# Kernel optimization log

Hardware: AMD Instinct MI355X
Metric: run time of the kernel (lower is better)

## Reference

```python
import jax, jax.numpy as jnp
import numpy as np

_EPS = 1e-4  # pytorch3d se3_exp_map clamps the SQUARED rotation angle at this eps


def _hat(w):
    # w: [..., 3] -> skew-symmetric [..., 3, 3]
    wx, wy, wz = w[..., 0], w[..., 1], w[..., 2]
    z = jnp.zeros_like(wx)
    return jnp.stack([
        jnp.stack([z, -wz, wy], axis=-1),
        jnp.stack([wz, z, -wx], axis=-1),
        jnp.stack([-wy, wx, z], axis=-1),
    ], axis=-2)


def _se3_exp(dofs):
    # dofs: [..., 6] = (log_translation, log_rotation), pytorch3d convention.
    # Returns R [..., 3, 3] and t [..., 3] such that p' = R @ p + t,
    # matching pytorch3d's row-convention matrix M ([:3,:3]=R^T, [3,:3]=t)
    # applied as p' = p @ M[:3,:3] + M[3,:3].
    t_log = dofs[..., :3]
    w = dofs[..., 3:]
    nrms = jnp.sum(w * w, axis=-1)
    theta = jnp.sqrt(jnp.clip(nrms, _EPS))  # [...]
    H = _hat(w)
    H2 = H @ H
    st, ct = jnp.sin(theta), jnp.cos(theta)
    f1 = (st / theta)[..., None, None]
    f2 = ((1.0 - ct) / (theta * theta))[..., None, None]
    f3 = ((theta - st) / (theta * theta * theta))[..., None, None]
    I = jnp.eye(3, dtype=dofs.dtype)
    R = I + f1 * H + f2 * H2            # Rodrigues
    V = I + f2 * H + f3 * H2            # left-Jacobian of SO(3)
    t = jnp.einsum('...ij,...j->...i', V, t_log)
    return R, t


def setup_inputs() -> dict:
    key = jax.random.key(0)
    k1, k2 = jax.random.split(key)
    B, T, N = 64, 28, 4096
    X_v = jax.random.normal(k1, (B, T, N, 3), dtype=jnp.float32)
    dofs = jax.random.normal(k2, (B, T, 6), dtype=jnp.float32)
    return {"X_v": X_v, "dofs": dofs}


def reference(X_v, dofs):
    # Fused, fully-batched version of the per-tooth python loop:
    # one SE3 exp over all (B,T) transforms + one batched point transform.
    R, t = _se3_exp(dofs)                                  # [B,T,3,3], [B,T,3]
    out = jnp.einsum('btij,btnj->btni', R, X_v) + t[:, :, None, :]
    return out
```

## Files before the change

### kernel.cpp

```cpp
#include <hip/hip_runtime.h>


typedef float f4 __attribute__((ext_vector_type(4)));

__device__ __forceinline__ float rfl(float x) {
    return __uint_as_float(__builtin_amdgcn_readfirstlane(__float_as_uint(x)));
}

__global__ __launch_bounds__(256) void se3_apply_kernel(
    const float* __restrict__ X,
    const float* __restrict__ dofs,
    float* __restrict__ out,
    int n3,
    int tilesPerBT)
{
    const int bt   = blockIdx.x / tilesPerBT;
    const int tile = blockIdx.x - bt * tilesPerBT;
    const int t    = threadIdx.x;

    const int fInBT = tile * 3072 + t * 12;
    const long long baseF = (long long)bt * (long long)n3 + (long long)fInBT;
    const f4* __restrict__ Xp = (const f4*)(X + baseF);
    f4* __restrict__ Op       = (f4*)(out + baseF);

    const bool full = (fInBT + 12) <= n3;
    f4 v0, v1, v2;
    if (full) { v0 = Xp[0]; v1 = Xp[1]; v2 = Xp[2]; }

    const float* d = dofs + bt * 6;
    const float tx = d[0], ty = d[1], tz = d[2];
    const float wx = d[3], wy = d[4], wz = d[5];

    const float nrm2  = wx * wx + wy * wy + wz * wz;
    const float th2   = fmaxf(nrm2, 1e-4f);
    const float theta = sqrtf(th2);
    const float st = sinf(theta);
    const float ct = cosf(theta);
    const float f1 = st / theta;
    const float f2 = (1.0f - ct) / th2;
    const float f3 = (theta - st) / (th2 * theta);

    const float xx = wx * wx, yy = wy * wy, zz = wz * wz;
    const float xy = wx * wy, xz = wx * wz, yz = wy * wz;

    const float R00 = rfl(1.0f - f2 * (yy + zz));
    const float R01 = rfl(f2 * xy - f1 * wz);
    const float R02 = rfl(f2 * xz + f1 * wy);
    const float R10 = rfl(f2 * xy + f1 * wz);
    const float R11 = rfl(1.0f - f2 * (xx + zz));
    const float R12 = rfl(f2 * yz - f1 * wx);
    const float R20 = rfl(f2 * xz - f1 * wy);
    const float R21 = rfl(f2 * yz + f1 * wx);
    const float R22 = rfl(1.0f - f2 * (xx + yy));

    const float V00 = 1.0f - f3 * (yy + zz);
    const float V01 = f3 * xy - f2 * wz;
    const float V02 = f3 * xz + f2 * wy;
    const float V10 = f3 * xy + f2 * wz;
    const float V11 = 1.0f - f3 * (xx + zz);
    const float V12 = f3 * yz - f2 * wx;
    const float V20 = f3 * xz - f2 * wy;
    const float V21 = f3 * yz + f2 * wx;
    const float V22 = 1.0f - f3 * (xx + yy);

    const float Tx = rfl(V00 * tx + V01 * ty + V02 * tz);
    const float Ty = rfl(V10 * tx + V11 * ty + V12 * tz);
    const float Tz = rfl(V20 * tx + V21 * ty + V22 * tz);

    if (full) {
        const float x0 = v0.x, y0 = v0.y, z0 = v0.z;
        const float x1 = v0.w, y1 = v1.x, z1 = v1.y;
        const float x2 = v1.z, y2 = v1.w, z2 = v2.x;
        const float x3 = v2.y, y3 = v2.z, z3 = v2.w;

        f4 o0, o1, o2;
        o0.x = fmaf(R00, x0, fmaf(R01, y0, fmaf(R02, z0, Tx)));
        o0.y = fmaf(R10, x0, fmaf(R11, y0, fmaf(R12, z0, Ty)));
        o0.z = fmaf(R20, x0, fmaf(R21, y0, fmaf(R22, z0, Tz)));
        o0.w = fmaf(R00, x1, fmaf(R01, y1, fmaf(R02, z1, Tx)));
        o1.x = fmaf(R10, x1, fmaf(R11, y1, fmaf(R12, z1, Ty)));
        o1.y = fmaf(R20, x1, fmaf(R21, y1, fmaf(R22, z1, Tz)));
        o1.z = fmaf(R00, x2, fmaf(R01, y2, fmaf(R02, z2, Tx)));
        o1.w = fmaf(R10, x2, fmaf(R11, y2, fmaf(R12, z2, Ty)));
        o2.x = fmaf(R20, x2, fmaf(R21, y2, fmaf(R22, z2, Tz)));
        o2.y = fmaf(R00, x3, fmaf(R01, y3, fmaf(R02, z3, Tx)));
        o2.z = fmaf(R10, x3, fmaf(R11, y3, fmaf(R12, z3, Ty)));
        o2.w = fmaf(R20, x3, fmaf(R21, y3, fmaf(R22, z3, Tz)));

        __builtin_nontemporal_store(o0, Op + 0);
        __builtin_nontemporal_store(o1, Op + 1);
        __builtin_nontemporal_store(o2, Op + 2);
    } else {
        const long long base = (long long)bt * (long long)n3;
        for (int f = fInBT; f + 3 <= n3; f += 3) {
            const float px = X[base + f + 0], py = X[base + f + 1], pz = X[base + f + 2];
            out[base + f + 0] = fmaf(R00, px, fmaf(R01, py, fmaf(R02, pz, Tx)));
            out[base + f + 1] = fmaf(R10, px, fmaf(R11, py, fmaf(R12, pz, Ty)));
            out[base + f + 2] = fmaf(R20, px, fmaf(R21, py, fmaf(R22, pz, Tz)));
        }
    }
}

extern "C" void kernel_launch(void* const* d_in, const int* in_sizes, int n_in,
                              void* d_out, int out_size, void* d_ws, size_t ws_size,
                              hipStream_t stream) {
    const float* X    = (const float*)d_in[0];
    const float* dofs = (const float*)d_in[1];
    float* out        = (float*)d_out;

    const int BT = in_sizes[1] / 6;
    const int n3 = in_sizes[0] / BT;

    const int tilesPerBT = (n3 + 3071) / 3072;

    dim3 grid((unsigned)(BT * tilesPerBT));
    se3_apply_kernel<<<grid, 256, 0, stream>>>(X, dofs, out, n3, tilesPerBT);
}
```

Baseline: 167.4 us.

## Split SE3 precompute into separate kernel and double per-thread work in streaming pass

Adds a small pre-kernel that computes each transform's rotation and translation once into workspace. A streaming kernel then reads those 12 floats per block instead of recomputing sin/cos in every block, and each thread handles 24 floats instead of 12. Nontemporal stores become plain stores, and the previous fused kernel is kept as a fallback when no workspace is available. The cost is an extra kernel launch and a dependent workspace read in exchange for less redundant per-block math.

```diff
diff --git a/kernel.cpp b/kernel.cpp
--- a/kernel.cpp
+++ b/kernel.cpp
@@ -3,31 +3,12 @@
 
 typedef float f4 __attribute__((ext_vector_type(4)));
 
-__device__ __forceinline__ float rfl(float x) {
-    return __uint_as_float(__builtin_amdgcn_readfirstlane(__float_as_uint(x)));
-}
-
-__global__ __launch_bounds__(256) void se3_apply_kernel(
-    const float* __restrict__ X,
-    const float* __restrict__ dofs,
-    float* __restrict__ out,
-    int n3,
-    int tilesPerBT)
+__global__ __launch_bounds__(256) void se3_pre(
+    const float* __restrict__ dofs, float* __restrict__ ws, int BT)
 {
-    const int bt   = blockIdx.x / tilesPerBT;
-    const int tile = blockIdx.x - bt * tilesPerBT;
-    const int t    = threadIdx.x;
-
-    const int fInBT = tile * 3072 + t * 12;
-    const long long baseF = (long long)bt * (long long)n3 + (long long)fInBT;
-    const f4* __restrict__ Xp = (const f4*)(X + baseF);
-    f4* __restrict__ Op       = (f4*)(out + baseF);
-
-    const bool full = (fInBT + 12) <= n3;
-    f4 v0, v1, v2;
-    if (full) { v0 = Xp[0]; v1 = Xp[1]; v2 = Xp[2]; }
-
-    const float* d = dofs + bt * 6;
+    const int i = blockIdx.x * 256 + threadIdx.x;
+    if (i >= BT) return;
+    const float* d = dofs + i * 6;
     const float tx = d[0], ty = d[1], tz = d[2];
     const float wx = d[3], wy = d[4], wz = d[5];
 
@@ -43,6 +24,120 @@
     const float xx = wx * wx, yy = wy * wy, zz = wz * wz;
     const float xy = wx * wy, xz = wx * wz, yz = wy * wz;
 
+    const float R00 = 1.0f - f2 * (yy + zz);
+    const float R01 = f2 * xy - f1 * wz;
+    const float R02 = f2 * xz + f1 * wy;
+    const float R10 = f2 * xy + f1 * wz;
+    const float R11 = 1.0f - f2 * (xx + zz);
+    const float R12 = f2 * yz - f1 * wx;
+    const float R20 = f2 * xz - f1 * wy;
+    const float R21 = f2 * yz + f1 * wx;
+    const float R22 = 1.0f - f2 * (xx + yy);
+
+    const float V00 = 1.0f - f3 * (yy + zz);
+    const float V01 = f3 * xy - f2 * wz;
+    const float V02 = f3 * xz + f2 * wy;
+    const float V10 = f3 * xy + f2 * wz;
+    const float V11 = 1.0f - f3 * (xx + zz);
+    const float V12 = f3 * yz - f2 * wx;
+    const float V20 = f3 * xz - f2 * wy;
+    const float V21 = f3 * yz + f2 * wx;
+    const float V22 = 1.0f - f3 * (xx + yy);
+
+    const float Tx = V00 * tx + V01 * ty + V02 * tz;
+    const float Ty = V10 * tx + V11 * ty + V12 * tz;
+    const float Tz = V20 * tx + V21 * ty + V22 * tz;
+
+    f4* W = (f4*)(ws + (long long)i * 16);
+    W[0] = (f4){R00, R01, R02, Tx};
+    W[1] = (f4){R10, R11, R12, Ty};
+    W[2] = (f4){R20, R21, R22, Tz};
+}
+
+__global__ __launch_bounds__(256) void se3_stream(
+    const float* __restrict__ X, const float* __restrict__ ws,
+    float* __restrict__ out, int n3, int tilesPerBT)
+{
+    const int bt   = blockIdx.x / tilesPerBT;
+    const int tile = blockIdx.x - bt * tilesPerBT;
+    const int t    = threadIdx.x;
+
+    const int fInBT = tile * 6144 + t * 24;
+    const long long baseF = (long long)bt * (long long)n3 + (long long)fInBT;
+    const f4* __restrict__ Xp = (const f4*)(X + baseF);
+    f4* __restrict__ Op       = (f4*)(out + baseF);
+
+    const bool full = (fInBT + 24) <= n3;
+    f4 v0, v1, v2, v3, v4, v5;
+    if (full) {
+        v0 = Xp[0]; v1 = Xp[1]; v2 = Xp[2];
+        v3 = Xp[3]; v4 = Xp[4]; v5 = Xp[5];
+    }
+
+    const f4* __restrict__ W = (const f4*)(ws + (long long)bt * 16);
+    const f4 w0 = W[0], w1 = W[1], w2 = W[2];
+
+    if (full) {
+        const float s[24] = {v0.x, v0.y, v0.z, v0.w, v1.x, v1.y, v1.z, v1.w,
+                             v2.x, v2.y, v2.z, v2.w, v3.x, v3.y, v3.z, v3.w,
+                             v4.x, v4.y, v4.z, v4.w, v5.x, v5.y, v5.z, v5.w};
+        float r[24];
+#pragma unroll
+        for (int k = 0; k < 8; ++k) {
+            const float x = s[3 * k], y = s[3 * k + 1], z = s[3 * k + 2];
+            r[3 * k]     = fmaf(w0.x, x, fmaf(w0.y, y, fmaf(w0.z, z, w0.w)));
+            r[3 * k + 1] = fmaf(w1.x, x, fmaf(w1.y, y, fmaf(w1.z, z, w1.w)));
+            r[3 * k + 2] = fmaf(w2.x, x, fmaf(w2.y, y, fmaf(w2.z, z, w2.w)));
+        }
+        Op[0] = (f4){r[0],  r[1],  r[2],  r[3]};
+        Op[1] = (f4){r[4],  r[5],  r[6],  r[7]};
+        Op[2] = (f4){r[8],  r[9],  r[10], r[11]};
+        Op[3] = (f4){r[12], r[13], r[14], r[15]};
+        Op[4] = (f4){r[16], r[17], r[18], r[19]};
+        Op[5] = (f4){r[20], r[21], r[22], r[23]};
+    } else {
+        const long long base = (long long)bt * (long long)n3;
+        for (int f = fInBT; f + 3 <= n3 && f < fInBT + 24; f += 3) {
+            const float px = X[base + f + 0], py = X[base + f + 1], pz = X[base + f + 2];
+            out[base + f + 0] = fmaf(w0.x, px, fmaf(w0.y, py, fmaf(w0.z, pz, w0.w)));
+            out[base + f + 1] = fmaf(w1.x, px, fmaf(w1.y, py, fmaf(w1.z, pz, w1.w)));
+            out[base + f + 2] = fmaf(w2.x, px, fmaf(w2.y, py, fmaf(w2.z, pz, w2.w)));
+        }
+    }
+}
+
+__device__ __forceinline__ float rfl(float x) {
+    return __uint_as_float(__builtin_amdgcn_readfirstlane(__float_as_uint(x)));
+}
+
+__global__ __launch_bounds__(256) void se3_apply_fused(
+    const float* __restrict__ X, const float* __restrict__ dofs,
+    float* __restrict__ out, int n3, int tilesPerBT)
+{
+    const int bt   = blockIdx.x / tilesPerBT;
+    const int tile = blockIdx.x - bt * tilesPerBT;
+    const int t    = threadIdx.x;
+    const int fInBT = tile * 3072 + t * 12;
+    const long long baseF = (long long)bt * (long long)n3 + (long long)fInBT;
+    const f4* __restrict__ Xp = (const f4*)(X + baseF);
+    f4* __restrict__ Op       = (f4*)(out + baseF);
+
+    const bool full = (fInBT + 12) <= n3;
+    f4 v0, v1, v2;
+    if (full) { v0 = Xp[0]; v1 = Xp[1]; v2 = Xp[2]; }
+
+    const float* d = dofs + bt * 6;
+    const float tx = d[0], ty = d[1], tz = d[2];
+    const float wx = d[3], wy = d[4], wz = d[5];
+    const float nrm2  = wx * wx + wy * wy + wz * wz;
+    const float th2   = fmaxf(nrm2, 1e-4f);
+    const float theta = sqrtf(th2);
+    const float st = sinf(theta), ct = cosf(theta);
+    const float f1 = st / theta;
+    const float f2 = (1.0f - ct) / th2;
+    const float f3 = (theta - st) / (th2 * theta);
+    const float xx = wx * wx, yy = wy * wy, zz = wz * wz;
+    const float xy = wx * wy, xz = wx * wz, yz = wy * wz;
     const float R00 = rfl(1.0f - f2 * (yy + zz));
     const float R01 = rfl(f2 * xy - f1 * wz);
     const float R02 = rfl(f2 * xz + f1 * wy);
@@ -52,7 +147,6 @@
     const float R20 = rfl(f2 * xz - f1 * wy);
     const float R21 = rfl(f2 * yz + f1 * wx);
     const float R22 = rfl(1.0f - f2 * (xx + yy));
-
     const float V00 = 1.0f - f3 * (yy + zz);
     const float V01 = f3 * xy - f2 * wz;
     const float V02 = f3 * xz + f2 * wy;
@@ -62,7 +156,6 @@
     const float V20 = f3 * xz - f2 * wy;
     const float V21 = f3 * yz + f2 * wx;
     const float V22 = 1.0f - f3 * (xx + yy);
-
     const float Tx = rfl(V00 * tx + V01 * ty + V02 * tz);
     const float Ty = rfl(V10 * tx + V11 * ty + V12 * tz);
     const float Tz = rfl(V20 * tx + V21 * ty + V22 * tz);
@@ -72,7 +165,6 @@
         const float x1 = v0.w, y1 = v1.x, z1 = v1.y;
         const float x2 = v1.z, y2 = v1.w, z2 = v2.x;
         const float x3 = v2.y, y3 = v2.z, z3 = v2.w;
-
         f4 o0, o1, o2;
         o0.x = fmaf(R00, x0, fmaf(R01, y0, fmaf(R02, z0, Tx)));
         o0.y = fmaf(R10, x0, fmaf(R11, y0, fmaf(R12, z0, Ty)));
@@ -86,13 +178,10 @@
         o2.y = fmaf(R00, x3, fmaf(R01, y3, fmaf(R02, z3, Tx)));
         o2.z = fmaf(R10, x3, fmaf(R11, y3, fmaf(R12, z3, Ty)));
         o2.w = fmaf(R20, x3, fmaf(R21, y3, fmaf(R22, z3, Tz)));
-
-        __builtin_nontemporal_store(o0, Op + 0);
-        __builtin_nontemporal_store(o1, Op + 1);
-        __builtin_nontemporal_store(o2, Op + 2);
+        Op[0] = o0; Op[1] = o1; Op[2] = o2;
     } else {
         const long long base = (long long)bt * (long long)n3;
-        for (int f = fInBT; f + 3 <= n3; f += 3) {
+        for (int f = fInBT; f + 3 <= n3 && f < fInBT + 12; f += 3) {
             const float px = X[base + f + 0], py = X[base + f + 1], pz = X[base + f + 2];
             out[base + f + 0] = fmaf(R00, px, fmaf(R01, py, fmaf(R02, pz, Tx)));
             out[base + f + 1] = fmaf(R10, px, fmaf(R11, py, fmaf(R12, pz, Ty)));
@@ -111,8 +200,18 @@
     const int BT = in_sizes[1] / 6;
     const int n3 = in_sizes[0] / BT;
 
-    const int tilesPerBT = (n3 + 3071) / 3072;
-
-    dim3 grid((unsigned)(BT * tilesPerBT));
-    se3_apply_kernel<<<grid, 256, 0, stream>>>(X, dofs, out, n3, tilesPerBT);
-}
+    const size_t wsNeed = (size_t)BT * 16 * sizeof(float);
+    if (d_ws != nullptr && ws_size >= wsNeed) {
+        float* ws = (float*)d_ws;
+        const int preBlocks = (BT + 255) / 256;
+        se3_pre<<<dim3((unsigned)preBlocks), 256, 0, stream>>>(dofs, ws, BT);
+
+        const int tilesPerBT = (n3 + 6143) / 6144;
+        dim3 grid((unsigned)(BT * tilesPerBT));
+        se3_stream<<<grid, 256, 0, stream>>>(X, ws, out, n3, tilesPerBT);
+    } else {
+        const int tilesPerBT = (n3 + 3071) / 3072;
+        dim3 grid((unsigned)(BT * tilesPerBT));
+        se3_apply_fused<<<grid, 256, 0, stream>>>(X, dofs, out, n3, tilesPerBT);
+    }
+}
```

Measured after the change: 167.0 us. Within noise of the previous version (-0.2%).
